# Kernel tuning notes

Hardware: AMD Instinct MI355X
Metric: run time of the kernel (lower is better)

Reference implementation:

```python
import jax, jax.numpy as jnp
import numpy as np

B, S, D = 4, 4096, 1024
H, WIN = 16, 256
DK = D // H
NW = S // WIN


def setup_inputs() -> dict:
    key = jax.random.key(0)
    ks = jax.random.split(key, 11)
    mk = lambda k, shape: jax.random.normal(k, shape, dtype=jnp.float32)
    w = lambda k: mk(k, (D, D)) * 0.02  # torch Linear weight [out, in]
    b = lambda k: mk(k, (D,)) * 0.02
    return {
        "query": mk(ks[0], (B, S, D)),
        "key": mk(ks[1], (B, S, D)),
        "value": mk(ks[2], (B, S, D)),
        "Wq": w(ks[3]), "bq": b(ks[4]),
        "Wk": w(ks[5]), "bk": b(ks[6]),
        "Wv": w(ks[7]), "bv": b(ks[8]),
        "Wo": w(ks[9]), "bo": b(ks[10]),
    }


def reference(query, key, value, Wq, bq, Wk, bk, Wv, bv, Wo, bo):
    scale = 1.0 / float(DK) ** 0.5

    def proj(x, Wm, bi):
        y = x @ Wm.T + bi
        return y.reshape(B, S, H, DK).transpose(0, 2, 1, 3).reshape(B, H, NW, WIN, DK)

    q = proj(query, Wq, bq)
    k = proj(key, Wk, bk)
    v = proj(value, Wv, bv)

    scores = jnp.einsum("bhnqd,bhnkd->bhnqk", q, k) * scale
    p_attn = jax.nn.softmax(scores, axis=-1)
    x = jnp.einsum("bhnqk,bhnkd->bhnqd", p_attn, v)

    # merge windows + heads -> [B,S,D], then output projection
    x = x.reshape(B, H, S, DK).transpose(0, 2, 1, 3).reshape(B, S, D)
    return x @ Wo.T + bo
```

## Files before the change

### kernel.cpp

```cpp
#include <hip/hip_runtime.h>
#include <hip/hip_bf16.h>

typedef __attribute__((ext_vector_type(8))) __bf16 bf16x8;
typedef __attribute__((ext_vector_type(4))) float f32x4;

#define DEVI static __device__ __forceinline__


DEVI ushort f2bf(float f) {
  unsigned u = __builtin_bit_cast(unsigned, f);
  return (ushort)((u + 0x7fffu + ((u >> 16) & 1u)) >> 16);
}

union BF8 { unsigned u[4]; bf16x8 v; };

DEVI bf16x8 cvt8(const float* __restrict__ p) {
  const f32x4 a = *(const f32x4*)p;
  const f32x4 b = *(const f32x4*)(p + 4);
  BF8 r;
  asm("v_cvt_pk_bf16_f32 %0, %1, %2" : "=v"(r.u[0]) : "v"(a.x), "v"(a.y));
  asm("v_cvt_pk_bf16_f32 %0, %1, %2" : "=v"(r.u[1]) : "v"(a.z), "v"(a.w));
  asm("v_cvt_pk_bf16_f32 %0, %1, %2" : "=v"(r.u[2]) : "v"(b.x), "v"(b.y));
  asm("v_cvt_pk_bf16_f32 %0, %1, %2" : "=v"(r.u[3]) : "v"(b.z), "v"(b.w));
  return r.v;
}

DEVI bf16x8 cvt8r(f32x4 a, f32x4 b) {
  BF8 r;
  asm("v_cvt_pk_bf16_f32 %0, %1, %2" : "=v"(r.u[0]) : "v"(a.x), "v"(a.y));
  asm("v_cvt_pk_bf16_f32 %0, %1, %2" : "=v"(r.u[1]) : "v"(a.z), "v"(a.w));
  asm("v_cvt_pk_bf16_f32 %0, %1, %2" : "=v"(r.u[2]) : "v"(b.x), "v"(b.y));
  asm("v_cvt_pk_bf16_f32 %0, %1, %2" : "=v"(r.u[3]) : "v"(b.z), "v"(b.w));
  return r.v;
}

DEVI void gload16(const void* g, void* l) {
  __builtin_amdgcn_global_load_lds(
      (const __attribute__((address_space(1))) unsigned*)g,
      (__attribute__((address_space(3))) unsigned*)l, 16, 0, 0);
}

DEVI int xcd_swizzle(int bid, int nwg) {
  return (bid & 7) * (nwg >> 3) + (bid >> 3);
}

DEVI f32x4 mfma16(bf16x8 a, bf16x8 b, f32x4 c) {
  return __builtin_amdgcn_mfma_f32_16x16x32_bf16(a, b, c, 0, 0, 0);
}


__global__ __launch_bounds__(256) void cvt_w(
    const float* __restrict__ wq, const float* __restrict__ wk,
    const float* __restrict__ wv, const float* __restrict__ wo,
    ushort* __restrict__ oq, ushort* __restrict__ ok2,
    ushort* __restrict__ ov, ushort* __restrict__ oo) {
  const int s = blockIdx.x >> 7;
  const int tb = blockIdx.x & 127;
  const float* src = s == 0 ? wq : (s == 1 ? wk : (s == 2 ? wv : wo));
  ushort* dst = s == 0 ? oq : (s == 1 ? ok2 : (s == 2 ? ov : oo));
  const unsigned G = 128 * 256;
  const unsigned t = tb * 256 + threadIdx.x;
#pragma unroll
  for (int j = 0; j < 4; ++j) {
    const size_t i = (size_t)t + (size_t)j * G;
    *(bf16x8*)(dst + i * 8) = cvt8(src + i * 8);
  }
}


template <int OUT>
__global__ __launch_bounds__(512, 2) void gemm_8ph(
    const ushort* __restrict__ A, const ushort* __restrict__ B,
    const float* __restrict__ bias, void* __restrict__ Cp, int N, int K) {
  __shared__ __align__(16) ushort Asm[4][8192];
  __shared__ __align__(16) ushort Bsm[4][8192];
  const int tid = threadIdx.x, lane = tid & 63;
  const int wv = tid >> 6;
  const int wr = wv >> 2, wc = wv & 3;
  const int cc = lane & 15, cr = lane >> 4;
  const int nw = N >> 8;
  const int work = xcd_swizzle(blockIdx.x, gridDim.x);
  const size_t m0 = (size_t)(work / nw) * 256;
  const size_t n0 = (size_t)(work % nw) * 256;

  const ushort *ag[2], *bg[2];
#pragma unroll
  for (int h = 0; h < 2; ++h) {
    const int u = tid + h * 512;
    const int row = u >> 2, slot = u & 3;
    const int gc = (slot ^ ((row >> 1) & 3)) * 8;
    ag[h] = A + (m0 + row) * (size_t)K + gc;
    bg[h] = B + (n0 + row) * (size_t)K + gc;
  }

  auto stageh = [&](int buf, int kt, int h) {
    gload16(ag[h] + kt, &Asm[buf][(tid + h * 512) * 8]);
    gload16(bg[h] + kt, &Bsm[buf][(tid + h * 512) * 8]);
  };

  f32x4 acc[8][4] = {};
  const int nt = K >> 5;

  int aoff[8], boff[4];
#pragma unroll
  for (int m = 0; m < 8; ++m) {
    const int row = wr * 128 + m * 16 + cc;
    aoff[m] = (row * 4 + (cr ^ ((row >> 1) & 3))) * 8;
  }
#pragma unroll
  for (int n = 0; n < 4; ++n) {
    const int row = wc * 64 + n * 16 + cc;
    boff[n] = (row * 4 + (cr ^ ((row >> 1) & 3))) * 8;
  }

#pragma unroll
  for (int p = 0; p < 3; ++p) {
    stageh(p, p << 5, 0);
    stageh(p, p << 5, 1);
  }
  asm volatile("s_waitcnt vmcnt(8)" ::: "memory");
  __builtin_amdgcn_s_barrier();
  asm volatile("" ::: "memory");

  for (int k = 0; k < nt; ++k) {
    const ushort* Ab = Asm[k & 3];
    const ushort* Bb = Bsm[k & 3];
    const int wb = (k + 3) & 3;
    const bool more = (k + 3 < nt);
    bf16x8 bf[4], af[4];

#pragma unroll
    for (int n = 0; n < 4; ++n) bf[n] = *(const bf16x8*)&Bb[boff[n]];
#pragma unroll
    for (int m = 0; m < 4; ++m) af[m] = *(const bf16x8*)&Ab[aoff[m]];
    if (more) stageh(wb, (k + 3) << 5, 0);
    __builtin_amdgcn_s_barrier();
    asm volatile("s_waitcnt lgkmcnt(0)" ::: "memory");
    __builtin_amdgcn_s_setprio(1);
#pragma unroll
    for (int m = 0; m < 4; ++m)
#pragma unroll
      for (int n = 0; n < 4; ++n)
        acc[m][n] = mfma16(af[m], bf[n], acc[m][n]);
    __builtin_amdgcn_s_setprio(0);
    asm volatile("" ::: "memory");
    __builtin_amdgcn_s_barrier();

#pragma unroll
    for (int m = 0; m < 4; ++m) af[m] = *(const bf16x8*)&Ab[aoff[4 + m]];
    if (more) stageh(wb, (k + 3) << 5, 1);
    if (k < nt - 3) {
      asm volatile("s_waitcnt vmcnt(8)" ::: "memory");
    } else if (k == nt - 3) {
      asm volatile("s_waitcnt vmcnt(4)" ::: "memory");
    } else if (k == nt - 2) {
      asm volatile("s_waitcnt vmcnt(0)" ::: "memory");
    }
    __builtin_amdgcn_s_barrier();
    asm volatile("s_waitcnt lgkmcnt(0)" ::: "memory");
    __builtin_amdgcn_s_setprio(1);
#pragma unroll
    for (int m = 0; m < 4; ++m)
#pragma unroll
      for (int n = 0; n < 4; ++n)
        acc[4 + m][n] = mfma16(af[m], bf[n], acc[4 + m][n]);
    __builtin_amdgcn_s_setprio(0);
    asm volatile("" ::: "memory");
    __builtin_amdgcn_s_barrier();
  }

#pragma unroll
  for (int n = 0; n < 4; ++n) {
    const size_t col = n0 + wc * 64 + n * 16 + cc;
    const float bval = bias[col];
#pragma unroll
    for (int m = 0; m < 8; ++m) {
      const size_t row0 = m0 + wr * 128 + m * 16 + cr * 4;
#pragma unroll
      for (int r = 0; r < 4; ++r) {
        const float val = acc[m][n][r] + bval;
        if constexpr (OUT == 0)
          ((float*)Cp)[(row0 + r) * N + col] = val;
        else if constexpr (OUT == 1)
          ((ushort*)Cp)[(row0 + r) * N + col] = f2bf(val);
        else
          ((ushort*)Cp)[col * 16384 + row0 + r] = f2bf(val);
      }
    }
  }
}


template <int OUT>
__global__ __launch_bounds__(512, 2) void gemm_8ph_f32a(
    const float* __restrict__ A, const ushort* __restrict__ B,
    const float* __restrict__ bias, void* __restrict__ Cp, int N, int K) {
  __shared__ __align__(16) ushort Asm[4][8192];
  __shared__ __align__(16) ushort Bsm[4][8192];
  const int tid = threadIdx.x, lane = tid & 63;
  const int wv = tid >> 6;
  const int wr = wv >> 2, wc = wv & 3;
  const int cc = lane & 15, cr = lane >> 4;
  const int nw = N >> 8;
  const int work = xcd_swizzle(blockIdx.x, gridDim.x);
  const size_t m0 = (size_t)(work / nw) * 256;
  const size_t n0 = (size_t)(work % nw) * 256;

  const float *af0, *af1;
  ushort *al0, *al1;
  {
    const int u0 = tid, r0 = u0 >> 2, s0 = u0 & 3;
    const int u1 = tid + 512, r1 = u1 >> 2, s1 = u1 & 3;
    af0 = A + (m0 + r0) * (size_t)K + (s0 ^ ((r0 >> 1) & 3)) * 8;
    af1 = A + (m0 + r1) * (size_t)K + (s1 ^ ((r1 >> 1) & 3)) * 8;
    al0 = &Asm[0][0] + u0 * 8;
    al1 = &Asm[0][0] + u1 * 8;
  }
  const ushort* bg[2];
#pragma unroll
  for (int h = 0; h < 2; ++h) {
    const int u = tid + h * 512;
    const int row = u >> 2, slot = u & 3;
    bg[h] = B + (n0 + row) * (size_t)K + (slot ^ ((row >> 1) & 3)) * 8;
  }

  f32x4 acc[8][4] = {};
  const int nt = K >> 5;

  int aoff[8], boff[4];
#pragma unroll
  for (int m = 0; m < 8; ++m) {
    const int row = wr * 128 + m * 16 + cc;
    aoff[m] = (row * 4 + (cr ^ ((row >> 1) & 3))) * 8;
  }
#pragma unroll
  for (int n = 0; n < 4; ++n) {
    const int row = wc * 64 + n * 16 + cc;
    boff[n] = (row * 4 + (cr ^ ((row >> 1) & 3))) * 8;
  }

  f32x4 sa0, sa1, sa2, sa3, sb0, sb1, sb2, sb3;
#pragma unroll
  for (int p = 0; p < 2; ++p) {
    const int kt = p << 5;
    sa0 = *(const f32x4*)(af0 + kt);  sa1 = *(const f32x4*)(af0 + kt + 4);
    sa2 = *(const f32x4*)(af1 + kt);  sa3 = *(const f32x4*)(af1 + kt + 4);
    *(bf16x8*)(al0 + p * 8192) = cvt8r(sa0, sa1);
    *(bf16x8*)(al1 + p * 8192) = cvt8r(sa2, sa3);
  }
  sa0 = *(const f32x4*)(af0 + 64);  sa1 = *(const f32x4*)(af0 + 68);
  sa2 = *(const f32x4*)(af1 + 64);  sa3 = *(const f32x4*)(af1 + 68);
#pragma unroll
  for (int p = 0; p < 3; ++p) {
    gload16(bg[0] + (p << 5), &Bsm[p][tid * 8]);
    gload16(bg[1] + (p << 5), &Bsm[p][(tid + 512) * 8]);
  }
  asm volatile("s_waitcnt vmcnt(0) lgkmcnt(0)" ::: "memory");
  __builtin_amdgcn_s_barrier();
  asm volatile("" ::: "memory");

#define F32A_TILE(k, W0, W1, W2, W3, L0, L1, L2, L3)                          \
  {                                                                           \
    const ushort* Ab = Asm[(k) & 3];                                          \
    const ushort* Bb = Bsm[(k) & 3];                                          \
    const int wb = ((k) + 3) & 3;                                             \
    const bool more = ((k) + 3 < nt);                                         \
    bf16x8 bf[4], af[4];                                                      \
    _Pragma("unroll")                                                         \
    for (int n = 0; n < 4; ++n) bf[n] = *(const bf16x8*)&Bb[boff[n]];         \
    _Pragma("unroll")                                                         \
    for (int m = 0; m < 4; ++m) af[m] = *(const bf16x8*)&Ab[aoff[m]];         \
    if (more) {                                                               \
      const int kt = ((k) + 3) << 5;                                          \
      L0 = *(const f32x4*)(af0 + kt);  L1 = *(const f32x4*)(af0 + kt + 4);    \
      L2 = *(const f32x4*)(af1 + kt);  L3 = *(const f32x4*)(af1 + kt + 4);    \
      gload16(bg[0] + kt, &Bsm[wb][tid * 8]);                                 \
    }                                                                         \
    if ((k) < nt - 3) {                                                       \
      asm volatile("s_waitcnt vmcnt(17)" ::: "memory");                       \
    } else if ((k) == nt - 3) {                                               \
      asm volatile("s_waitcnt vmcnt(12)" ::: "memory");                       \
    } else if ((k) == nt - 2) {                                               \
      asm volatile("s_waitcnt vmcnt(6)" ::: "memory");                        \
    } else {                                                                  \
      asm volatile("s_waitcnt vmcnt(0)" ::: "memory");                        \
    }                                                                         \
    __builtin_amdgcn_s_barrier();                                             \
    asm volatile("s_waitcnt lgkmcnt(0)" ::: "memory");                        \
    __builtin_amdgcn_s_setprio(1);                                            \
    _Pragma("unroll")                                                         \
    for (int m = 0; m < 4; ++m)                                               \
      _Pragma("unroll")                                                       \
      for (int n = 0; n < 4; ++n) acc[m][n] = mfma16(af[m], bf[n], acc[m][n]);\
    __builtin_amdgcn_s_setprio(0);                                            \
    asm volatile("" ::: "memory");                                            \
    __builtin_amdgcn_s_barrier();                                             \
    _Pragma("unroll")                                                         \
    for (int m = 0; m < 4; ++m) af[m] = *(const bf16x8*)&Ab[aoff[4 + m]];     \
    if (more) gload16(bg[1] + (((k) + 3) << 5), &Bsm[wb][(tid + 512) * 8]);   \
    __builtin_amdgcn_s_barrier();                                             \
    asm volatile("s_waitcnt lgkmcnt(0)" ::: "memory");                        \
    __builtin_amdgcn_s_setprio(1);                                            \
    _Pragma("unroll")                                                         \
    for (int m = 0; m < 4; ++m)                                               \
      _Pragma("unroll")                                                       \
      for (int n = 0; n < 4; ++n)                                             \
        acc[4 + m][n] = mfma16(af[m], bf[n], acc[4 + m][n]);                  \
    __builtin_amdgcn_s_setprio(0);                                            \
    if ((k) + 2 < nt) {       \
      const int wbuf = ((k) + 2) & 3;                                         \
      *(bf16x8*)(al0 + wbuf * 8192) = cvt8r(W0, W1);                          \
      *(bf16x8*)(al1 + wbuf * 8192) = cvt8r(W2, W3);                          \
    }                                                                         \
    asm volatile("s_waitcnt lgkmcnt(0)" ::: "memory");                        \
    __builtin_amdgcn_s_barrier();                                             \
  }

  for (int kk = 0; kk < nt; kk += 2) {
    F32A_TILE(kk, sa0, sa1, sa2, sa3, sb0, sb1, sb2, sb3);
    F32A_TILE(kk + 1, sb0, sb1, sb2, sb3, sa0, sa1, sa2, sa3);
  }
#undef F32A_TILE

#pragma unroll
  for (int n = 0; n < 4; ++n) {
    const size_t col = n0 + wc * 64 + n * 16 + cc;
    const float bval = bias[col];
#pragma unroll
    for (int m = 0; m < 8; ++m) {
      const size_t row0 = m0 + wr * 128 + m * 16 + cr * 4;
#pragma unroll
      for (int r = 0; r < 4; ++r) {
        const float val = acc[m][n][r] + bval;
        if constexpr (OUT == 1)
          ((ushort*)Cp)[(row0 + r) * N + col] = f2bf(val);
        else
          ((ushort*)Cp)[col * 16384 + row0 + r] = f2bf(val);
      }
    }
  }
}


__global__ __launch_bounds__(512) void attn_kernel(
    const ushort* __restrict__ q, const ushort* __restrict__ k,
    const ushort* __restrict__ vt, ushort* __restrict__ x) {
  __shared__ __align__(16) ushort Ks[256 * 64];
  __shared__ __align__(16) ushort Vt[64 * 256];
  __shared__ ushort Pw[8][16 * 264];
  const int bid = blockIdx.x;
  const int w = bid & 15, h = (bid >> 4) & 15, b = bid >> 8;
  const int tid = threadIdx.x, lane = tid & 63, wv = tid >> 6;
  const int cc = lane & 15, cr = lane >> 4;
  const size_t base = ((size_t)b * 4096 + (size_t)w * 256) * 1024 + h * 64;
  const size_t vbase = ((size_t)h * 64) * 16384 + (size_t)b * 4096 + w * 256;

#pragma unroll
  for (int i = 0; i < 4; ++i) {
    const int u = tid + i * 512;
    const int row = u >> 3, slot = u & 7;
    gload16(k + base + (size_t)row * 1024 + ((slot ^ (row & 7)) << 3),
            &Ks[u * 8]);
  }
#pragma unroll
  for (int i = 0; i < 4; ++i) {
    const int u = tid + i * 512;
    const int dk = u >> 5, slot = u & 31;
    gload16(vt + vbase + (size_t)dk * 16384 + (((slot & 24) | ((slot ^ dk) & 7)) << 3),
            &Vt[u * 8]);
  }
  __syncthreads();

  ushort* Pp = Pw[wv];
  for (int c = 0; c < 2; ++c) {
    const int qrow0 = wv * 32 + c * 16;
    const ushort* qp = q + base + (size_t)(qrow0 + cc) * 1024 + cr * 8;
    const bf16x8 qf0 = *(const bf16x8*)qp;
    const bf16x8 qf1 = *(const bf16x8*)(qp + 32);

    f32x4 sc[16];
#pragma unroll
    for (int cb = 0; cb < 16; ++cb) {
      const int row = cb * 16 + cc;
      const bf16x8 kb0 = *(const bf16x8*)&Ks[row * 64 + ((cr ^ (row & 7)) << 3)];
      const bf16x8 kb1 =
          *(const bf16x8*)&Ks[row * 64 + (((4 + cr) ^ (row & 7)) << 3)];
      f32x4 z = {0.f, 0.f, 0.f, 0.f};
      z = mfma16(qf0, kb0, z);
      z = mfma16(qf1, kb1, z);
      sc[cb] = z;
    }

    float inv[4];
#pragma unroll
    for (int r = 0; r < 4; ++r) {
      float mx = -1e30f;
#pragma unroll
      for (int cb = 0; cb < 16; ++cb) mx = fmaxf(mx, sc[cb][r]);
      mx = fmaxf(mx, __shfl_xor(mx, 1));
      mx = fmaxf(mx, __shfl_xor(mx, 2));
      mx = fmaxf(mx, __shfl_xor(mx, 4));
      mx = fmaxf(mx, __shfl_xor(mx, 8));
      float sum = 0.f;
#pragma unroll
      for (int cb = 0; cb < 16; ++cb) {
        const float p = __expf((sc[cb][r] - mx) * 0.125f);
        sc[cb][r] = p;
        sum += p;
      }
      sum += __shfl_xor(sum, 1);
      sum += __shfl_xor(sum, 2);
      sum += __shfl_xor(sum, 4);
      sum += __shfl_xor(sum, 8);
      inv[r] = 1.f / sum;
    }

#pragma unroll
    for (int r = 0; r < 4; ++r)
#pragma unroll
      for (int cb = 0; cb < 16; ++cb)
        Pp[(cr * 4 + r) * 264 + cb * 16 + cc] = f2bf(sc[cb][r]);

    bf16x8 pf[8];
#pragma unroll
    for (int ks = 0; ks < 8; ++ks)
      pf[ks] = *(const bf16x8*)&Pp[cc * 264 + ks * 32 + cr * 8];
    f32x4 o[4] = {};
#pragma unroll
    for (int db = 0; db < 4; ++db) {
      const int row = db * 16 + cc;
#pragma unroll
      for (int ks = 0; ks < 8; ++ks) {
        const int gu = ks * 4 + cr;
        const int lu = (gu & 24) | ((gu ^ row) & 7);
        const bf16x8 bv = *(const bf16x8*)&Vt[row * 256 + lu * 8];
        o[db] = mfma16(pf[ks], bv, o[db]);
      }
    }

#pragma unroll
    for (int db = 0; db < 4; ++db)
#pragma unroll
      for (int r = 0; r < 4; ++r) {
        const int qr = qrow0 + cr * 4 + r;
        x[base + (size_t)qr * 1024 + db * 16 + cc] = f2bf(o[db][r] * inv[r]);
      }
  }
}


extern "C" void kernel_launch(void* const* d_in, const int* in_sizes, int n_in,
                              void* d_out, int out_size, void* d_ws, size_t ws_size,
                              hipStream_t stream) {
  const float* query = (const float*)d_in[0];
  const float* key_  = (const float*)d_in[1];
  const float* value = (const float*)d_in[2];
  const float* Wq = (const float*)d_in[3];
  const float* bq = (const float*)d_in[4];
  const float* Wk = (const float*)d_in[5];
  const float* bk = (const float*)d_in[6];
  const float* Wv = (const float*)d_in[7];
  const float* bv = (const float*)d_in[8];
  const float* Wo = (const float*)d_in[9];
  const float* bo = (const float*)d_in[10];
  float* out = (float*)d_out;

  const size_t MN = (size_t)16384 * 1024;
  const size_t WN = (size_t)1024 * 1024;
  ushort* wqb = (ushort*)d_ws;
  ushort* wkb = wqb + WN;
  ushort* wvb = wkb + WN;
  ushort* wob = wvb + WN;
  ushort* qp = wob + WN;
  ushort* kp = qp + MN;
  ushort* vtp = kp + MN;

  const dim3 b256(256), b512(512);
  const dim3 ggrid(64 * 4);

  cvt_w<<<dim3(4 * 128), b256, 0, stream>>>(Wq, Wk, Wv, Wo, wqb, wkb, wvb, wob);

  gemm_8ph_f32a<1><<<ggrid, b512, 0, stream>>>(query, wqb, bq, qp, 1024, 1024);
  gemm_8ph_f32a<1><<<ggrid, b512, 0, stream>>>(key_,  wkb, bk, kp, 1024, 1024);
  gemm_8ph_f32a<2><<<ggrid, b512, 0, stream>>>(value, wvb, bv, vtp, 1024, 1024);

  attn_kernel<<<dim3(1024), b512, 0, stream>>>(qp, kp, vtp, qp );

  gemm_8ph<0><<<ggrid, b512, 0, stream>>>(qp, wob, bo, out, 1024, 1024);
}
```

Baseline: 277.6 us.

## Merge Q/K/V projection GEMMs into one launch and tune attention kernel

```diff
diff --git a/kernel.cpp b/kernel.cpp
--- a/kernel.cpp
+++ b/kernel.cpp
@@ -32,6 +32,12 @@
   asm("v_cvt_pk_bf16_f32 %0, %1, %2" : "=v"(r.u[2]) : "v"(b.x), "v"(b.y));
   asm("v_cvt_pk_bf16_f32 %0, %1, %2" : "=v"(r.u[3]) : "v"(b.z), "v"(b.w));
   return r.v;
+}
+
+DEVI unsigned cvtpk1(float lo, float hi) {
+  unsigned r;
+  asm("v_cvt_pk_bf16_f32 %0, %1, %2" : "=v"(r) : "v"(lo), "v"(hi));
+  return r;
 }
 
 DEVI void gload16(const void* g, void* l) {
@@ -191,18 +197,28 @@
 }
 
 
-template <int OUT>
-__global__ __launch_bounds__(512, 2) void gemm_8ph_f32a(
-    const float* __restrict__ A, const ushort* __restrict__ B,
-    const float* __restrict__ bias, void* __restrict__ Cp, int N, int K) {
+__global__ __launch_bounds__(512, 2) void gemm_qkv(
+    const float* __restrict__ Aq, const float* __restrict__ Ak,
+    const float* __restrict__ Av, const ushort* __restrict__ Bq,
+    const ushort* __restrict__ Bk, const ushort* __restrict__ Bv,
+    const float* __restrict__ bq, const float* __restrict__ bk,
+    const float* __restrict__ bv, ushort* __restrict__ Cq,
+    ushort* __restrict__ Ck, ushort* __restrict__ Cv, int N, int K) {
   __shared__ __align__(16) ushort Asm[4][8192];
   __shared__ __align__(16) ushort Bsm[4][8192];
+  const int s = blockIdx.x >> 8;
+  const float* A = s == 0 ? Aq : (s == 1 ? Ak : Av);
+  const ushort* B = s == 0 ? Bq : (s == 1 ? Bk : Bv);
+  const float* bias = s == 0 ? bq : (s == 1 ? bk : bv);
+  ushort* Cp = s == 0 ? Cq : (s == 1 ? Ck : Cv);
+  const bool outT = (s == 2);
+
   const int tid = threadIdx.x, lane = tid & 63;
   const int wv = tid >> 6;
   const int wr = wv >> 2, wc = wv & 3;
   const int cc = lane & 15, cr = lane >> 4;
   const int nw = N >> 8;
-  const int work = xcd_swizzle(blockIdx.x, gridDim.x);
+  const int work = xcd_swizzle(blockIdx.x & 255, 256);
   const size_t m0 = (size_t)(work / nw) * 256;
   const size_t n0 = (size_t)(work % nw) * 256;
 
@@ -307,7 +323,7 @@
       for (int n = 0; n < 4; ++n)                                             \
         acc[4 + m][n] = mfma16(af[m], bf[n], acc[4 + m][n]);                  \
     __builtin_amdgcn_s_setprio(0);                                            \
-    if ((k) + 2 < nt) {       \
+    if ((k) + 2 < nt) {                                                       \
       const int wbuf = ((k) + 2) & 3;                                         \
       *(bf16x8*)(al0 + wbuf * 8192) = cvt8r(W0, W1);                          \
       *(bf16x8*)(al1 + wbuf * 8192) = cvt8r(W2, W3);                          \
@@ -332,10 +348,10 @@
 #pragma unroll
       for (int r = 0; r < 4; ++r) {
         const float val = acc[m][n][r] + bval;
-        if constexpr (OUT == 1)
-          ((ushort*)Cp)[(row0 + r) * N + col] = f2bf(val);
+        if (outT)
+          Cp[col * 16384 + row0 + r] = f2bf(val);
         else
-          ((ushort*)Cp)[col * 16384 + row0 + r] = f2bf(val);
+          Cp[(row0 + r) * N + col] = f2bf(val);
       }
     }
   }
@@ -355,6 +371,13 @@
   const size_t base = ((size_t)b * 4096 + (size_t)w * 256) * 1024 + h * 64;
   const size_t vbase = ((size_t)h * 64) * 16384 + (size_t)b * 4096 + w * 256;
 
+  const ushort* qp0 = q + base + (size_t)(wv * 32 + cc) * 1024 + cr * 8;
+  const ushort* qp1 = q + base + (size_t)(wv * 32 + 16 + cc) * 1024 + cr * 8;
+  const bf16x8 qA0 = *(const bf16x8*)qp0;
+  const bf16x8 qA1 = *(const bf16x8*)(qp0 + 32);
+  const bf16x8 qB0 = *(const bf16x8*)qp1;
+  const bf16x8 qB1 = *(const bf16x8*)(qp1 + 32);
+
 #pragma unroll
   for (int i = 0; i < 4; ++i) {
     const int u = tid + i * 512;
@@ -374,11 +397,11 @@
   ushort* Pp = Pw[wv];
   for (int c = 0; c < 2; ++c) {
     const int qrow0 = wv * 32 + c * 16;
-    const ushort* qp = q + base + (size_t)(qrow0 + cc) * 1024 + cr * 8;
-    const bf16x8 qf0 = *(const bf16x8*)qp;
-    const bf16x8 qf1 = *(const bf16x8*)(qp + 32);
+    const bf16x8 qf0 = c == 0 ? qA0 : qB0;
+    const bf16x8 qf1 = c == 0 ? qA1 : qB1;
 
     f32x4 sc[16];
+    __builtin_amdgcn_s_setprio(1);
 #pragma unroll
     for (int cb = 0; cb < 16; ++cb) {
       const int row = cb * 16 + cc;
@@ -390,6 +413,7 @@
       z = mfma16(qf1, kb1, z);
       sc[cb] = z;
     }
+    __builtin_amdgcn_s_setprio(0);
 
     float inv[4];
 #pragma unroll
@@ -416,16 +440,22 @@
     }
 
 #pragma unroll
-    for (int r = 0; r < 4; ++r)
-#pragma unroll
-      for (int cb = 0; cb < 16; ++cb)
-        Pp[(cr * 4 + r) * 264 + cb * 16 + cc] = f2bf(sc[cb][r]);
+    for (int r = 0; r < 4; ++r) {
+      ushort* prow = &Pp[(cr * 4 + r) * 264 + cc];
+#pragma unroll
+      for (int cb = 0; cb < 16; cb += 2) {
+        const unsigned pk = cvtpk1(sc[cb][r], sc[cb + 1][r]);
+        prow[cb * 16] = (ushort)pk;
+        prow[(cb + 1) * 16] = (ushort)(pk >> 16);
+      }
+    }
 
     bf16x8 pf[8];
 #pragma unroll
     for (int ks = 0; ks < 8; ++ks)
       pf[ks] = *(const bf16x8*)&Pp[cc * 264 + ks * 32 + cr * 8];
     f32x4 o[4] = {};
+    __builtin_amdgcn_s_setprio(1);
 #pragma unroll
     for (int db = 0; db < 4; ++db) {
       const int row = db * 16 + cc;
@@ -437,6 +467,7 @@
         o[db] = mfma16(pf[ks], bv, o[db]);
       }
     }
+    __builtin_amdgcn_s_setprio(0);
 
 #pragma unroll
     for (int db = 0; db < 4; ++db)
@@ -476,15 +507,13 @@
   ushort* vtp = kp + MN;
 
   const dim3 b256(256), b512(512);
-  const dim3 ggrid(64 * 4);
 
   cvt_w<<<dim3(4 * 128), b256, 0, stream>>>(Wq, Wk, Wv, Wo, wqb, wkb, wvb, wob);
 
-  gemm_8ph_f32a<1><<<ggrid, b512, 0, stream>>>(query, wqb, bq, qp, 1024, 1024);
-  gemm_8ph_f32a<1><<<ggrid, b512, 0, stream>>>(key_,  wkb, bk, kp, 1024, 1024);
-  gemm_8ph_f32a<2><<<ggrid, b512, 0, stream>>>(value, wvb, bv, vtp, 1024, 1024);
+  gemm_qkv<<<dim3(768), b512, 0, stream>>>(query, key_, value, wqb, wkb, wvb,
+                                           bq, bk, bv, qp, kp, vtp, 1024, 1024);
 
   attn_kernel<<<dim3(1024), b512, 0, stream>>>(qp, kp, vtp, qp );
 
-  gemm_8ph<0><<<ggrid, b512, 0, stream>>>(qp, wob, bo, out, 1024, 1024);
-}
+  gemm_8ph<0><<<dim3(256), b512, 0, stream>>>(qp, wob, bo, out, 1024, 1024);
+}
```

Measured after the change: 293.9 us. 1.06x slower.
